# Performance work log

Hardware: AMD Instinct MI355X
Metric: run time of the kernel (lower is better)

Reference implementation:

```python
import jax, jax.numpy as jnp
import numpy as np

N = 100000      # nodes
E = 1600000     # edges (avg degree 16)
IN = 128        # in_channels
HID = 128       # hidden_channels
OUT = 2         # out_channels
NEG_SLOPE = 0.2  # PyG GATConv default


def setup_inputs() -> dict:
    key = jax.random.key(0)
    ks = jax.random.split(key, 20)
    inp = {
        "x": jax.random.normal(ks[0], (N, IN), dtype=jnp.float32),
        "edge_index": jax.random.randint(ks[1], (2, E), 0, N, dtype=jnp.int32),
    }
    # GATConv params (heads=1): W:[din,dout], attention vecs a_src/a_dst:[dout], bias:[dout]
    dims = [(IN, HID), (HID, HID), (HID, HID)]
    for i, (din, dout) in enumerate(dims, start=1):
        base = 4 * i
        inp[f"W{i}"] = jax.random.normal(ks[base], (din, dout), dtype=jnp.float32) * (1.0 / np.sqrt(din))
        inp[f"a{i}s"] = jax.random.normal(ks[base + 1], (dout,), dtype=jnp.float32) * 0.1
        inp[f"a{i}d"] = jax.random.normal(ks[base + 2], (dout,), dtype=jnp.float32) * 0.1
        inp[f"b{i}"] = jnp.zeros((dout,), dtype=jnp.float32)
    inp["Wc"] = jax.random.normal(ks[16], (HID, OUT), dtype=jnp.float32) * (1.0 / np.sqrt(HID))
    inp["bc"] = jnp.zeros((OUT,), dtype=jnp.float32)
    return inp


def _gat_layer(x, src, dst, W, a_s, a_d, b, n):
    # Linear transform: [n, dout]
    h = x @ W
    # Edge attention logits: alpha_src[j] + alpha_dst[i], LeakyReLU (PyG GATConv)
    e = jax.nn.leaky_relu(jnp.take(h @ a_s, src) + jnp.take(h @ a_d, dst), NEG_SLOPE)
    # Stable softmax over incoming edges per destination node
    m = jax.ops.segment_max(e, dst, num_segments=n)
    ex = jnp.exp(e - m[dst])
    denom = jax.ops.segment_sum(ex, dst, num_segments=n)
    alpha = ex / denom[dst]
    # Weighted scatter-aggregation of source features into destinations
    out = jax.ops.segment_sum(alpha[:, None] * jnp.take(h, src, axis=0), dst, num_segments=n)
    return out + b


def reference(x, edge_index, W1, a1s, a1d, b1, W2, a2s, a2d, b2, W3, a3s, a3d, b3, Wc, bc):
    n = x.shape[0]
    # PyG GATConv default add_self_loops=True
    loop = jnp.arange(n, dtype=edge_index.dtype)
    src = jnp.concatenate([edge_index[0], loop])
    dst = jnp.concatenate([edge_index[1], loop])
    for (W, a_s, a_d, b) in ((W1, a1s, a1d, b1), (W2, a2s, a2d, b2), (W3, a3s, a3d, b3)):
        x = jax.nn.relu(_gat_layer(x, src, dst, W, a_s, a_d, b, n))
    return x @ Wc + bc
```

## Files before the change

kernel.cpp:

```cpp
#include <hip/hip_runtime.h>
#include <hip/hip_fp16.h>

#define NNODES 100000
#define NEDGES 1600000
#define DIM 128
#define NB ((NNODES + 63) / 64)
#define NCH 128
#define CHUNK ((NEDGES + NCH - 1) / NCH)
#define EBUF 2560
#define LSTR 136
#define NGR32 ((size_t)NNODES * 32)
#define CSRSZ (NEDGES + NB * 256 + 64)

typedef _Float16 f16x8 __attribute__((ext_vector_type(8)));
typedef float f32x4 __attribute__((ext_vector_type(4)));

__device__ __forceinline__ float leaky02(float t) { return t > 0.f ? t : 0.2f * t; }

union H8u  { uint2 u; __half2 h[2]; };
union H16u { uint4 u; __half2 h[4]; };


__global__ __launch_bounds__(256) void wprep(const float* __restrict__ W0,
                                             const float* __restrict__ W1,
                                             const float* __restrict__ W2,
                                             __half* __restrict__ wt) {
    int idx = blockIdx.x * 256 + threadIdx.x;
    if (idx >= 3 * 128 * 128) return;
    int l = idx >> 14, rem = idx & 16383;
    int nn = rem >> 7, k = rem & 127;
    const float* W = (l == 0) ? W0 : ((l == 1) ? W1 : W2);
    wt[idx] = __float2half_rn(W[k * 128 + nn]);
}

template <bool XF16>
__global__ __launch_bounds__(256) void gemm_mfma(const float* __restrict__ X,
                                                 const __half* __restrict__ X16,
                                                 const __half* __restrict__ wt16,
                                                 const float* __restrict__ as_,
                                                 const float* __restrict__ ad_,
                                                 __half* __restrict__ H,
                                                 float* __restrict__ s,
                                                 float* __restrict__ d, int n) {
    __shared__ __half As[64][LSTR];
    __shared__ __half Wt[128][LSTR];
    int t = threadIdx.x;
    int brow = blockIdx.x * 64;

    if (XF16) {
        for (int i = t; i < 64 * 16; i += 256) {
            int r = i >> 4, c8 = (i & 15) * 8;
            int gr = brow + r;
            int g = c8 >> 5, off = c8 & 31;
            uint4 v = (gr < n) ? *(const uint4*)(X16 + (size_t)g * NGR32 + (size_t)gr * 32 + off)
                               : make_uint4(0u, 0u, 0u, 0u);
            *(uint4*)&As[r][c8] = v;
        }
    } else {
        for (int i = t; i < 64 * 32; i += 256) {
            int r = i >> 5, c4 = (i & 31) * 4;
            int gr = brow + r;
            float4 v = (gr < n) ? *(const float4*)(X + (size_t)gr * 128 + c4)
                                : make_float4(0.f, 0.f, 0.f, 0.f);
            As[r][c4 + 0] = __float2half_rn(v.x);
            As[r][c4 + 1] = __float2half_rn(v.y);
            As[r][c4 + 2] = __float2half_rn(v.z);
            As[r][c4 + 3] = __float2half_rn(v.w);
        }
    }
    for (int i = t; i < 128 * 16; i += 256) {
        int r = i >> 4, c8 = (i & 15) * 8;
        *(uint4*)&Wt[r][c8] = *(const uint4*)(wt16 + r * 128 + c8);
    }
    __syncthreads();

    int wid  = t >> 6;
    int lane = t & 63;
    int lrow = lane & 15;
    int lkg  = lane >> 4;
    int r0   = wid * 16;

    f32x4 acc[8] = {};
#pragma unroll
    for (int kk = 0; kk < 128; kk += 32) {
        f16x8 af = *(const f16x8*)&As[r0 + lrow][kk + lkg * 8];
#pragma unroll
        for (int ct = 0; ct < 8; ++ct) {
            f16x8 bf = *(const f16x8*)&Wt[ct * 16 + lrow][kk + lkg * 8];
            acc[ct] = __builtin_amdgcn_mfma_f32_16x16x32_f16(af, bf, acc[ct], 0, 0, 0);
        }
    }

    float sp[4] = {0.f, 0.f, 0.f, 0.f};
    float dp[4] = {0.f, 0.f, 0.f, 0.f};
#pragma unroll
    for (int ct = 0; ct < 8; ++ct) {
        float a_s = as_[ct * 16 + lrow];
        float a_d = ad_[ct * 16 + lrow];
#pragma unroll
        for (int j = 0; j < 4; ++j) {
            sp[j] += acc[ct][j] * a_s;
            dp[j] += acc[ct][j] * a_d;
        }
    }
#pragma unroll
    for (int j = 0; j < 4; ++j) {
        int gr = brow + r0 + lkg * 4 + j;
        if (gr < n) {
#pragma unroll
            for (int ct = 0; ct < 8; ++ct)
                H[(size_t)(ct >> 1) * NGR32 + (size_t)gr * 32 + (ct & 1) * 16 + lrow] =
                    __float2half_rn(acc[ct][j]);
        }
    }
#pragma unroll
    for (int off = 1; off < 16; off <<= 1)
#pragma unroll
        for (int j = 0; j < 4; ++j) {
            sp[j] += __shfl_xor(sp[j], off);
            dp[j] += __shfl_xor(dp[j], off);
        }
    if (lrow == 0)
#pragma unroll
        for (int j = 0; j < 4; ++j) {
            int gr = brow + r0 + lkg * 4 + j;
            if (gr < n) { s[gr] = sp[j]; d[gr] = dp[j]; }
        }
}

__global__ __launch_bounds__(512) void bucket_count(const int* __restrict__ dst,
                                                    int* __restrict__ blockcounts) {
    __shared__ int hist[NB];
    int b = blockIdx.x, t = threadIdx.x;
    for (int i = t; i < NB; i += 512) hist[i] = 0;
    __syncthreads();
    int e0 = b * CHUNK, e1 = min(NEDGES, e0 + CHUNK);
    for (int e = e0 + t; e < e1; e += 512)
        atomicAdd(&hist[dst[e] >> 6], 1);
    __syncthreads();
    for (int i = t; i < NB; i += 512)
        blockcounts[i * NCH + b] = hist[i];
}

__global__ __launch_bounds__(NCH) void bucket_scan_a(int* __restrict__ blockcounts,
                                                     int* __restrict__ btotal) {
    int bin = blockIdx.x, t = threadIdx.x;
    int v = blockcounts[bin * NCH + t];
    int incl = v;
#pragma unroll
    for (int off = 1; off < 64; off <<= 1) {
        int u = __shfl_up(incl, off, 64);
        if ((t & 63) >= off) incl += u;
    }
    __shared__ int wsum;
    if (t == 63) wsum = incl;
    __syncthreads();
    int excl = incl - v + ((t >= 64) ? wsum : 0);
    blockcounts[bin * NCH + t] = excl;
    if (t == NCH - 1) btotal[bin] = excl + v;
}

__global__ __launch_bounds__(1024) void bucket_scan_b(const int* __restrict__ btotal,
                                                      int* __restrict__ bbase) {
    __shared__ int ts[2][1024];
    int t = threadIdx.x;
    int b0 = t * 2;
    int c0 = (b0 < NB)     ? btotal[b0]     : 0;
    int c1 = (b0 + 1 < NB) ? btotal[b0 + 1] : 0;
    int sum = c0 + c1;
    ts[0][t] = sum;
    __syncthreads();
    int sb = 0;
    for (int off = 1; off < 1024; off <<= 1) {
        int v = ts[sb][t] + ((t >= off) ? ts[sb][t - off] : 0);
        ts[sb ^ 1][t] = v;
        sb ^= 1;
        __syncthreads();
    }
    int excl = ts[sb][t] - sum;
    if (b0 < NB)     bbase[b0]     = excl;
    if (b0 + 1 < NB) bbase[b0 + 1] = excl + c0;
    if (t == 1023) bbase[NB] = ts[sb][1023];
}

__global__ __launch_bounds__(512) void bucket_scatter(const int* __restrict__ src,
                                                      const int* __restrict__ dst,
                                                      const int* __restrict__ blockcounts,
                                                      const int* __restrict__ bbase,
                                                      int* __restrict__ packed) {
    __shared__ int cur[NB];
    int b = blockIdx.x, t = threadIdx.x;
    for (int i = t; i < NB; i += 512) cur[i] = bbase[i] + blockcounts[i * NCH + b];
    __syncthreads();
    int e0 = b * CHUNK, e1 = min(NEDGES, e0 + CHUNK);
    for (int e = e0 + t; e < e1; e += 512) {
        int dv = dst[e];
        int bin = dv >> 6;
        int p = atomicAdd(&cur[bin], 1);
        packed[p] = ((dv & 63) << 17) | src[e];
    }
}

__global__ __launch_bounds__(256) void bucket_csr(const int* __restrict__ packed,
                                                  const int* __restrict__ bbase,
                                                  int* __restrict__ rowptr4,
                                                  int* __restrict__ cnts,
                                                  int* __restrict__ csr_src) {
    __shared__ int ebuf[EBUF];
    __shared__ int hist[64], cur[64];
    int i = blockIdx.x, t = threadIdx.x;
    int base_in = bbase[i], cnt = bbase[i + 1] - base_in;
    int pbase = ((base_in + 3) & ~3) + i * 256;
    bool inl = (cnt <= EBUF);
    if (inl) for (int j = t; j < cnt; j += 256) ebuf[j] = packed[base_in + j];
    if (t < 64) hist[t] = 0;
    __syncthreads();
    for (int j = t; j < cnt; j += 256) {
        int v = inl ? ebuf[j] : packed[base_in + j];
        atomicAdd(&hist[v >> 17], 1);
    }
    __syncthreads();
    if (t < 64) {
        int node = i * 64 + t;
        bool valid = node < NNODES;
        int h = hist[t];
        int c  = h + (valid ? 1 : 0);
        int c4 = (c + 3) & ~3;
        int incl = c4;
#pragma unroll
        for (int off = 1; off < 64; off <<= 1) {
            int u = __shfl_up(incl, off, 64);
            if (t >= off) incl += u;
        }
        int ex4 = incl - c4;
        cur[t] = pbase + ex4;
        if (valid) {
            rowptr4[node] = pbase + ex4;
            cnts[node] = c;
            csr_src[pbase + ex4 + h] = node;
        }
    }
    __syncthreads();
    for (int j = t; j < cnt; j += 256) {
        int v = inl ? ebuf[j] : packed[base_in + j];
        int off = atomicAdd(&cur[v >> 17], 1);
        csr_src[off] = v & 0x1FFFF;
    }
}

__global__ __launch_bounds__(256) void gat_alpha(const int* __restrict__ rowptr4,
                                                 const int* __restrict__ cnts,
                                                 const int* __restrict__ csr,
                                                 const float* __restrict__ s,
                                                 const float* __restrict__ d,
                                                 unsigned* __restrict__ packed2, int n) {
    int node = blockIdx.x * 8 + (threadIdx.x >> 5);
    if (node >= n) return;
    int lane = threadIdx.x & 31;
    int base = rowptr4[node];
    int cnt  = cnts[node];
    int cnt4 = (cnt + 3) & ~3;
    float dnode = d[node];

    if (cnt <= 32) {
        int si = csr[base + min(lane, cnt - 1)];
        float lv = leaky02(s[si] + dnode);
        float lm = (lane < cnt) ? lv : -1e30f;
#pragma unroll
        for (int off = 16; off; off >>= 1) lm = fmaxf(lm, __shfl_xor(lm, off));
        float w = (lane < cnt) ? expf(lv - lm) : 0.f;
        float denom = w;
#pragma unroll
        for (int off = 16; off; off >>= 1) denom += __shfl_xor(denom, off);
        if (lane < cnt)
            packed2[base + lane] = ((unsigned)si << 15) |
                                   (unsigned)__float2int_rn(w / denom * 32767.f);
        else if (lane < cnt4)
            packed2[base + lane] = (unsigned)node << 15;
    } else {
        float m = -1e30f;
        for (int c = 0; c < cnt; c += 32) {
            int idx = c + lane;
            float lv = (idx < cnt) ? leaky02(s[csr[base + idx]] + dnode) : -1e30f;
            m = fmaxf(m, lv);
        }
#pragma unroll
        for (int off = 16; off; off >>= 1) m = fmaxf(m, __shfl_xor(m, off));
        float denom = 0.f;
        for (int c = 0; c < cnt; c += 32) {
            int idx = c + lane;
            if (idx < cnt) denom += expf(leaky02(s[csr[base + idx]] + dnode) - m);
        }
#pragma unroll
        for (int off = 16; off; off >>= 1) denom += __shfl_xor(denom, off);
        for (int c = 0; c < cnt4; c += 32) {
            int idx = c + lane;
            if (idx < cnt) {
                int si = csr[base + idx];
                float w = expf(leaky02(s[si] + dnode) - m);
                packed2[base + idx] = ((unsigned)si << 15) |
                                      (unsigned)__float2int_rn(w / denom * 32767.f);
            } else if (idx < cnt4) {
                packed2[base + idx] = (unsigned)node << 15;
            }
        }
    }
}

__global__ __launch_bounds__(256) void gat_agg(const int* __restrict__ rowptr4,
                                               const int* __restrict__ cnts,
                                               const unsigned* __restrict__ packed2,
                                               const __half* __restrict__ H,
                                               const float* __restrict__ bias,
                                               __half* __restrict__ A16, int n) {
    int grp = blockIdx.x & 3;
    int blk = blockIdx.x >> 2;
    int wid = threadIdx.x >> 6;
    int lane = threadIdx.x & 63;
    int nd = lane >> 2;
    int cg = lane & 3;
    int node = blk * 64 + wid * 16 + nd;
    if (node >= n) return;
    const __half* Hs = H + (size_t)grp * NGR32 + cg * 8;
    __half* As = A16 + (size_t)grp * NGR32;

    int base  = rowptr4[node];
    int iters = (cnts[node] + 3) >> 2;
    const uint4* p = (const uint4*)(packed2 + base);
    float acc[8] = {0.f, 0.f, 0.f, 0.f, 0.f, 0.f, 0.f, 0.f};
    uint4 q = p[0];
    for (int it = 0; it < iters; ++it) {
        uint4 nq = p[it + 1];
        float a0 = (float)(q.x & 0x7fffu);
        float a1 = (float)(q.y & 0x7fffu);
        float a2 = (float)(q.z & 0x7fffu);
        float a3 = (float)(q.w & 0x7fffu);
        H16u h0, h1, h2, h3;
        h0.u = *(const uint4*)(Hs + (size_t)(q.x >> 15) * 32);
        h1.u = *(const uint4*)(Hs + (size_t)(q.y >> 15) * 32);
        h2.u = *(const uint4*)(Hs + (size_t)(q.z >> 15) * 32);
        h3.u = *(const uint4*)(Hs + (size_t)(q.w >> 15) * 32);
#pragma unroll
        for (int c2 = 0; c2 < 4; ++c2) {
            float2 f0 = __half22float2(h0.h[c2]);
            float2 f1 = __half22float2(h1.h[c2]);
            float2 f2 = __half22float2(h2.h[c2]);
            float2 f3 = __half22float2(h3.h[c2]);
            acc[c2 * 2 + 0] += a0 * f0.x + a1 * f1.x + a2 * f2.x + a3 * f3.x;
            acc[c2 * 2 + 1] += a0 * f0.y + a1 * f1.y + a2 * f2.y + a3 * f3.y;
        }
        q = nq;
    }
    const float scale = 1.f / 32767.f;
    int cb = grp * 32 + cg * 8;
    H16u pk16;
#pragma unroll
    for (int c2 = 0; c2 < 4; ++c2) {
        float o0 = fmaxf(acc[c2 * 2 + 0] * scale + bias[cb + c2 * 2 + 0], 0.f);
        float o1 = fmaxf(acc[c2 * 2 + 1] * scale + bias[cb + c2 * 2 + 1], 0.f);
        pk16.h[c2] = __floats2half2_rn(o0, o1);
    }
    *(uint4*)(As + (size_t)node * 32 + cg * 8) = pk16.u;
}

__global__ __launch_bounds__(256) void classify16(const __half* __restrict__ A,
                                                  const float* __restrict__ Wc,
                                                  const float* __restrict__ bc,
                                                  float* __restrict__ out, int n) {
    int node = blockIdx.x * 4 + (threadIdx.x >> 6);
    if (node >= n) return;
    int lane = threadIdx.x & 63;
    int col = lane * 2;
    int g = col >> 5, off = col & 31;
    __half2 h2 = *(const __half2*)(A + (size_t)g * NGR32 + (size_t)node * 32 + off);
    float2 f = __half22float2(h2);
    float o0 = f.x * Wc[col * 2]       + f.y * Wc[(col + 1) * 2];
    float o1 = f.x * Wc[col * 2 + 1]   + f.y * Wc[(col + 1) * 2 + 1];
#pragma unroll
    for (int offx = 32; offx; offx >>= 1) {
        o0 += __shfl_xor(o0, offx);
        o1 += __shfl_xor(o1, offx);
    }
    if (lane == 0) {
        out[(size_t)node * 2 + 0] = o0 + bc[0];
        out[(size_t)node * 2 + 1] = o1 + bc[1];
    }
}

extern "C" void kernel_launch(void* const* d_in, const int* in_sizes, int n_in,
                              void* d_out, int out_size, void* d_ws, size_t ws_size,
                              hipStream_t stream) {
    const float* x   = (const float*)d_in[0];
    const int*   ei  = (const int*)d_in[1];
    const int*   src = ei;
    const int*   dst = ei + NEDGES;
    const float* Ws[3]  = {(const float*)d_in[2], (const float*)d_in[6], (const float*)d_in[10]};
    const float* ass[3] = {(const float*)d_in[3], (const float*)d_in[7], (const float*)d_in[11]};
    const float* ads[3] = {(const float*)d_in[4], (const float*)d_in[8], (const float*)d_in[12]};
    const float* bs[3]  = {(const float*)d_in[5], (const float*)d_in[9], (const float*)d_in[13]};
    const float* Wc = (const float*)d_in[14];
    const float* bc = (const float*)d_in[15];
    float* out = (float*)d_out;

    const int n = NNODES;

    __half*   h16  = (__half*)d_ws;
    __half*   a16  = h16 + (size_t)n * DIM;
    __half*   wt16 = a16 + (size_t)n * DIM;
    float*    sbuf = (float*)(wt16 + 3 * 128 * 128);
    float*    dbuf = sbuf + n;
    int*      rowptr4     = (int*)(dbuf + n);
    int*      cnts        = rowptr4 + n;
    int*      csr_src     = cnts + n;
    unsigned* packed2     = (unsigned*)(csr_src + CSRSZ);
    int*      packed      = (int*)(packed2 + CSRSZ);
    int*      blockcounts = packed + NEDGES;
    int*      bbase       = blockcounts + NB * NCH;
    int*      btotal      = bbase + NB + 1;

    const int g64        = (n + 63) / 64;
    const int alpha_grid = (n + 7) / 8;
    const int cls_grid   = (n + 3) / 4;
    const int agg_grid   = ((n + 63) / 64) * 4;

    wprep<<<192, 256, 0, stream>>>(Ws[0], Ws[1], Ws[2], wt16);
    bucket_count<<<NCH, 512, 0, stream>>>(dst, blockcounts);
    bucket_scan_a<<<NB, NCH, 0, stream>>>(blockcounts, btotal);
    bucket_scan_b<<<1, 1024, 0, stream>>>(btotal, bbase);
    bucket_scatter<<<NCH, 512, 0, stream>>>(src, dst, blockcounts, bbase, packed);
    bucket_csr<<<NB, 256, 0, stream>>>(packed, bbase, rowptr4, cnts, csr_src);

    for (int layer = 0; layer < 3; ++layer) {
        const __half* wl = wt16 + (size_t)layer * 128 * 128;
        if (layer == 0)
            gemm_mfma<false><<<g64, 256, 0, stream>>>(x, a16, wl, ass[0], ads[0],
                                                      h16, sbuf, dbuf, n);
        else
            gemm_mfma<true><<<g64, 256, 0, stream>>>(x, a16, wl, ass[layer], ads[layer],
                                                     h16, sbuf, dbuf, n);
        gat_alpha<<<alpha_grid, 256, 0, stream>>>(rowptr4, cnts, csr_src, sbuf, dbuf,
                                                  packed2, n);
        gat_agg<<<agg_grid, 256, 0, stream>>>(rowptr4, cnts, packed2, h16, bs[layer], a16, n);
    }
    classify16<<<cls_grid, 256, 0, stream>>>(a16, Wc, bc, out, n);
}
```

Baseline: 403.1 us.

## Split neighbor aggregation into two source-half passes for cache locality

Each node's CSR edge list is partitioned into low-half and high-half source segments, each padded to a multiple of four. Aggregation runs in two kernel passes, one per half. The intent is to shrink the gathered H working set per pass so it fits better in L2/MALL cache. The cost is an extra launch, extra padding entries, and a round trip of the partial sum through fp16 storage between passes, which slightly reduces accuracy.

```diff
diff --git a/kernel.cpp b/kernel.cpp
--- a/kernel.cpp
+++ b/kernel.cpp
@@ -2,6 +2,7 @@
 #include <hip/hip_fp16.h>
 
 #define NNODES 100000
+#define NHALF 50000
 #define NEDGES 1600000
 #define DIM 128
 #define NB ((NNODES + 63) / 64)
@@ -10,7 +11,7 @@
 #define EBUF 2560
 #define LSTR 136
 #define NGR32 ((size_t)NNODES * 32)
-#define CSRSZ (NEDGES + NB * 256 + 64)
+#define CSRSZ (NEDGES + NB * 512 + 64)
 
 typedef _Float16 f16x8 __attribute__((ext_vector_type(8)));
 typedef float f32x4 __attribute__((ext_vector_type(4)));
@@ -207,44 +208,53 @@
                                                   int* __restrict__ cnts,
                                                   int* __restrict__ csr_src) {
     __shared__ int ebuf[EBUF];
-    __shared__ int hist[64], cur[64];
+    __shared__ int hist[64], histL[64], curL[64], curH[64];
     int i = blockIdx.x, t = threadIdx.x;
     int base_in = bbase[i], cnt = bbase[i + 1] - base_in;
-    int pbase = ((base_in + 3) & ~3) + i * 256;
+    int pbase = ((base_in + 3) & ~3) + i * 512;
     bool inl = (cnt <= EBUF);
     if (inl) for (int j = t; j < cnt; j += 256) ebuf[j] = packed[base_in + j];
-    if (t < 64) hist[t] = 0;
+    if (t < 64) { hist[t] = 0; histL[t] = 0; }
     __syncthreads();
     for (int j = t; j < cnt; j += 256) {
         int v = inl ? ebuf[j] : packed[base_in + j];
-        atomicAdd(&hist[v >> 17], 1);
+        int t64 = v >> 17;
+        atomicAdd(&hist[t64], 1);
+        if ((v & 0x1FFFF) < NHALF) atomicAdd(&histL[t64], 1);
     }
     __syncthreads();
     if (t < 64) {
         int node = i * 64 + t;
         bool valid = node < NNODES;
-        int h = hist[t];
-        int c  = h + (valid ? 1 : 0);
-        int c4 = (c + 3) & ~3;
-        int incl = c4;
+        int h = hist[t], hl = histL[t];
+        bool selfLow = valid && (node < NHALF);
+        int cl = hl + (selfLow ? 1 : 0);
+        int ch = (h - hl) + ((valid && !selfLow) ? 1 : 0);
+        int c4l = (cl + 3) & ~3, c4h = (ch + 3) & ~3;
+        int tot4 = c4l + c4h;
+        int incl = tot4;
 #pragma unroll
         for (int off = 1; off < 64; off <<= 1) {
             int u = __shfl_up(incl, off, 64);
             if (t >= off) incl += u;
         }
-        int ex4 = incl - c4;
-        cur[t] = pbase + ex4;
+        int ex = incl - tot4;
+        int nodebase = pbase + ex;
+        curL[t] = nodebase;
+        curH[t] = nodebase + c4l;
         if (valid) {
-            rowptr4[node] = pbase + ex4;
-            cnts[node] = c;
-            csr_src[pbase + ex4 + h] = node;
+            rowptr4[node] = nodebase;
+            cnts[node] = cl | (ch << 16);
+            csr_src[selfLow ? (nodebase + hl) : (nodebase + c4l + (h - hl))] = node;
         }
     }
     __syncthreads();
     for (int j = t; j < cnt; j += 256) {
         int v = inl ? ebuf[j] : packed[base_in + j];
-        int off = atomicAdd(&cur[v >> 17], 1);
-        csr_src[off] = v & 0x1FFFF;
+        int t64 = v >> 17;
+        int srcv = v & 0x1FFFF;
+        int off = (srcv < NHALF) ? atomicAdd(&curL[t64], 1) : atomicAdd(&curH[t64], 1);
+        csr_src[off] = srcv;
     }
 }
 
@@ -258,55 +268,69 @@
     if (node >= n) return;
     int lane = threadIdx.x & 31;
     int base = rowptr4[node];
-    int cnt  = cnts[node];
-    int cnt4 = (cnt + 3) & ~3;
+    int cw = cnts[node];
+    int cl = cw & 0xFFFF, ch = cw >> 16;
+    int c4l = (cl + 3) & ~3, c4h = (ch + 3) & ~3;
+    int tot = c4l + c4h;
     float dnode = d[node];
 
-    if (cnt <= 32) {
-        int si = csr[base + min(lane, cnt - 1)];
-        float lv = leaky02(s[si] + dnode);
-        float lm = (lane < cnt) ? lv : -1e30f;
+    if (tot <= 32) {
+        bool real = (lane < cl) || (lane >= c4l && lane < c4l + ch);
+        int si = real ? csr[base + lane] : 0;
+        float lv = real ? leaky02(s[si] + dnode) : -1e30f;
+        float lm = lv;
 #pragma unroll
         for (int off = 16; off; off >>= 1) lm = fmaxf(lm, __shfl_xor(lm, off));
-        float w = (lane < cnt) ? expf(lv - lm) : 0.f;
+        float w = real ? expf(lv - lm) : 0.f;
         float denom = w;
 #pragma unroll
         for (int off = 16; off; off >>= 1) denom += __shfl_xor(denom, off);
-        if (lane < cnt)
-            packed2[base + lane] = ((unsigned)si << 15) |
-                                   (unsigned)__float2int_rn(w / denom * 32767.f);
-        else if (lane < cnt4)
-            packed2[base + lane] = (unsigned)node << 15;
+        if (lane < tot) {
+            unsigned pk = real ? (((unsigned)si << 15) |
+                                  (unsigned)__float2int_rn(w / denom * 32767.f))
+                               : (lane < c4l ? 0u : ((unsigned)NHALF << 15));
+            packed2[base + lane] = pk;
+        }
     } else {
         float m = -1e30f;
-        for (int c = 0; c < cnt; c += 32) {
+        for (int c = 0; c < tot; c += 32) {
             int idx = c + lane;
-            float lv = (idx < cnt) ? leaky02(s[csr[base + idx]] + dnode) : -1e30f;
+            bool real = (idx < cl) || (idx >= c4l && idx < c4l + ch);
+            int si = real ? csr[base + idx] : 0;
+            float lv = real ? leaky02(s[si] + dnode) : -1e30f;
             m = fmaxf(m, lv);
         }
 #pragma unroll
         for (int off = 16; off; off >>= 1) m = fmaxf(m, __shfl_xor(m, off));
         float denom = 0.f;
-        for (int c = 0; c < cnt; c += 32) {
+        for (int c = 0; c < tot; c += 32) {
             int idx = c + lane;
-            if (idx < cnt) denom += expf(leaky02(s[csr[base + idx]] + dnode) - m);
+            bool real = (idx < cl) || (idx >= c4l && idx < c4l + ch);
+            int si = real ? csr[base + idx] : 0;
+            if (real) denom += expf(leaky02(s[si] + dnode) - m);
         }
 #pragma unroll
         for (int off = 16; off; off >>= 1) denom += __shfl_xor(denom, off);
-        for (int c = 0; c < cnt4; c += 32) {
+        for (int c = 0; c < tot; c += 32) {
             int idx = c + lane;
-            if (idx < cnt) {
-                int si = csr[base + idx];
-                float w = expf(leaky02(s[si] + dnode) - m);
-                packed2[base + idx] = ((unsigned)si << 15) |
-                                      (unsigned)__float2int_rn(w / denom * 32767.f);
-            } else if (idx < cnt4) {
-                packed2[base + idx] = (unsigned)node << 15;
+            if (idx < tot) {
+                bool real = (idx < cl) || (idx >= c4l && idx < c4l + ch);
+                int si = real ? csr[base + idx] : 0;
+                unsigned pk;
+                if (real) {
+                    float w = expf(leaky02(s[si] + dnode) - m);
+                    pk = ((unsigned)si << 15) |
+                         (unsigned)__float2int_rn(w / denom * 32767.f);
+                } else {
+                    pk = (idx < c4l) ? 0u : ((unsigned)NHALF << 15);
+                }
+                packed2[base + idx] = pk;
             }
         }
     }
 }
 
+template <int PASS>
 __global__ __launch_bounds__(256) void gat_agg(const int* __restrict__ rowptr4,
                                                const int* __restrict__ cnts,
                                                const unsigned* __restrict__ packed2,
@@ -324,9 +348,17 @@
     const __half* Hs = H + (size_t)grp * NGR32 + cg * 8;
     __half* As = A16 + (size_t)grp * NGR32;
 
-    int base  = rowptr4[node];
-    int iters = (cnts[node] + 3) >> 2;
-    const uint4* p = (const uint4*)(packed2 + base);
+    int base = rowptr4[node];
+    int cw   = cnts[node];
+    int cl = cw & 0xFFFF, ch = cw >> 16;
+    int iters, off0;
+    if (PASS == 0) { iters = (cl + 3) >> 2; off0 = 0; }
+    else           { iters = (ch + 3) >> 2; off0 = (cl + 3) & ~3; }
+    const uint4* p = (const uint4*)(packed2 + base + off0);
+
+    H16u part;
+    if (PASS == 1) part.u = *(const uint4*)(As + (size_t)node * 32 + cg * 8);
+
     float acc[8] = {0.f, 0.f, 0.f, 0.f, 0.f, 0.f, 0.f, 0.f};
     uint4 q = p[0];
     for (int it = 0; it < iters; ++it) {
@@ -352,13 +384,21 @@
         q = nq;
     }
     const float scale = 1.f / 32767.f;
-    int cb = grp * 32 + cg * 8;
     H16u pk16;
-#pragma unroll
-    for (int c2 = 0; c2 < 4; ++c2) {
-        float o0 = fmaxf(acc[c2 * 2 + 0] * scale + bias[cb + c2 * 2 + 0], 0.f);
-        float o1 = fmaxf(acc[c2 * 2 + 1] * scale + bias[cb + c2 * 2 + 1], 0.f);
-        pk16.h[c2] = __floats2half2_rn(o0, o1);
+    if (PASS == 0) {
+#pragma unroll
+        for (int c2 = 0; c2 < 4; ++c2)
+            pk16.h[c2] = __floats2half2_rn(acc[c2 * 2 + 0] * scale,
+                                           acc[c2 * 2 + 1] * scale);
+    } else {
+        int cb = grp * 32 + cg * 8;
+#pragma unroll
+        for (int c2 = 0; c2 < 4; ++c2) {
+            float2 pv = __half22float2(part.h[c2]);
+            float o0 = fmaxf(pv.x + acc[c2 * 2 + 0] * scale + bias[cb + c2 * 2 + 0], 0.f);
+            float o1 = fmaxf(pv.y + acc[c2 * 2 + 1] * scale + bias[cb + c2 * 2 + 1], 0.f);
+            pk16.h[c2] = __floats2half2_rn(o0, o1);
+        }
     }
     *(uint4*)(As + (size_t)node * 32 + cg * 8) = pk16.u;
 }
@@ -440,7 +480,8 @@
                                                      h16, sbuf, dbuf, n);
         gat_alpha<<<alpha_grid, 256, 0, stream>>>(rowptr4, cnts, csr_src, sbuf, dbuf,
                                                   packed2, n);
-        gat_agg<<<agg_grid, 256, 0, stream>>>(rowptr4, cnts, packed2, h16, bs[layer], a16, n);
+        gat_agg<0><<<agg_grid, 256, 0, stream>>>(rowptr4, cnts, packed2, h16, bs[layer], a16, n);
+        gat_agg<1><<<agg_grid, 256, 0, stream>>>(rowptr4, cnts, packed2, h16, bs[layer], a16, n);
     }
     classify16<<<cls_grid, 256, 0, stream>>>(a16, Wc, bc, out, n);
 }
```

Measured after the change: 377.4 us. -6.4%, faster.
